# Kernel tuning notes

Hardware: AMD Instinct MI355X
Metric: run time of the kernel (lower is better)

Reference implementation:

```python
import jax, jax.numpy as jnp
import numpy as np

B, T, N, F = 4, 1, 12500, 64
C = 64        # spatial_hidden_dim (heads=1)
OUT = 64      # spatial_out_features
E = 1600000
NT = B * N    # total flattened nodes


def setup_inputs() -> dict:
    key = jax.random.key(0)
    ks = jax.random.split(key, 12)
    s = lambda d: 1.0 / np.sqrt(d)
    return {
        "x": jax.random.normal(ks[0], (B, T, N, F), jnp.float32),
        "edge_index": jax.random.randint(ks[1], (2, E), 0, NT, jnp.int64),
        "edge_attr": jax.random.uniform(ks[2], (E, 1), jnp.float32),
        "W_l": jax.random.normal(ks[3], (F, C), jnp.float32) * s(F),
        "b_l": jnp.zeros((C,), jnp.float32),
        "W_r": jax.random.normal(ks[4], (F, C), jnp.float32) * s(F),
        "b_r": jnp.zeros((C,), jnp.float32),
        "W_e": jax.random.normal(ks[5], (1, C), jnp.float32),
        "att": jax.random.normal(ks[6], (C,), jnp.float32) * s(C),
        "bias": jnp.zeros((C,), jnp.float32),
        "W_fc": jax.random.normal(ks[7], (C, OUT), jnp.float32) * s(C),
        "b_fc": jnp.zeros((OUT,), jnp.float32),
    }


def reference(x, edge_index, edge_attr, W_l, b_l, W_r, b_r, W_e, att, bias, W_fc, b_fc):
    Bx, Tx, Nx, Fx = x.shape
    x2 = x.reshape(Bx * Nx, Fx)                      # [NT, F] (requires T==1)
    xl = x2 @ W_l + b_l                              # [NT, C] source transform
    xr = x2 @ W_r + b_r                              # [NT, C] target transform
    src, dst = edge_index[0], edge_index[1]
    e = edge_attr @ W_e                              # [E, C] lin_edge (no bias)
    m = jax.nn.leaky_relu(xl[src] + xr[dst] + e, 0.2)  # [E, C]
    score = m @ att                                  # [E]
    # segment softmax over destination nodes
    smax = jax.lax.stop_gradient(jax.ops.segment_max(score, dst, num_segments=Bx * Nx))
    ex = jnp.exp(score - smax[dst])
    denom = jax.ops.segment_sum(ex, dst, num_segments=Bx * Nx)
    alpha = ex / denom[dst]                          # [E]
    agg = jax.ops.segment_sum(alpha[:, None] * xl[src], dst, num_segments=Bx * Nx)
    out = (agg + bias).reshape(Bx, Nx, -1)           # [B, N, C]
    return out @ W_fc + b_fc                         # [B, N, OUT]
```

## Files before the change

kernel.cpp:

```cpp
#include <hip/hip_runtime.h>
#include <math.h>

#define LRELU(v) ((v) >= 0.f ? (v) : 0.2f * (v))

#define NB_SHIFT 4
#define BKT_NODES 16
#define MAXB 768
#define MAX_NBKT 3200
#define BIN_CHUNK 16384
#define TR_BLOCKS 512

__device__ __forceinline__ unsigned short f32_to_bf16_rne(float f) {
    unsigned int b = __float_as_uint(f);
    b += 0x7FFFu + ((b >> 16) & 1u);
    return (unsigned short)(b >> 16);
}

__global__ void __launch_bounds__(256) k_prep(
    const float* __restrict__ x,
    const float* __restrict__ W_l, const float* __restrict__ b_l,
    const float* __restrict__ W_r, const float* __restrict__ b_r,
    unsigned short* __restrict__ xl16, float* __restrict__ xr,
    const int* __restrict__ ei, const float* __restrict__ ea,
    int* __restrict__ bcnt, int2* __restrict__ bucket,
    int NT, int E, int nbkt, int binBlocks)
{
    __shared__ __align__(16) char smem[33792];
    const int t = threadIdx.x;
    if ((int)blockIdx.x < binBlocks) {
        int* lh = (int*)smem;
        int* lb = lh + MAX_NBKT;
        const int e0 = (int)blockIdx.x * BIN_CHUNK;
        const int e1 = (e0 + BIN_CHUNK < E) ? e0 + BIN_CHUNK : E;
        const int n = e1 - e0;
        const int nv4 = n >> 2;
        const int4* d4 = (const int4*)(ei + E + e0);
        const int4* s4 = (const int4*)(ei + e0);
        const float4* a4 = (const float4*)(ea + e0);
        for (int i = t; i < nbkt; i += 256) lh[i] = 0;
        __syncthreads();
        for (int j = t; j < nv4; j += 256) {
            const int4 v = d4[j];
            atomicAdd(&lh[v.x >> NB_SHIFT], 1);
            atomicAdd(&lh[v.y >> NB_SHIFT], 1);
            atomicAdd(&lh[v.z >> NB_SHIFT], 1);
            atomicAdd(&lh[v.w >> NB_SHIFT], 1);
        }
        for (int j = e0 + (nv4 << 2) + t; j < e1; j += 256)
            atomicAdd(&lh[ei[E + j] >> NB_SHIFT], 1);
        __syncthreads();
        for (int i = t; i < nbkt; i += 256) {
            const int c = lh[i];
            lb[i] = c ? atomicAdd(&bcnt[i], c) : 0;
            lh[i] = 0;
        }
        __syncthreads();
        for (int j = t; j < nv4; j += 256) {
            const int4 dv = d4[j];
            const int4 sv = s4[j];
            const float4 av = a4[j];
            int bkt, pos;
            bkt = dv.x >> NB_SHIFT;
            pos = lb[bkt] + atomicAdd(&lh[bkt], 1);
            if (pos < MAXB) bucket[(size_t)bkt * MAXB + pos] =
                make_int2(__float_as_int(av.x), sv.x | ((dv.x & (BKT_NODES - 1)) << 16));
            bkt = dv.y >> NB_SHIFT;
            pos = lb[bkt] + atomicAdd(&lh[bkt], 1);
            if (pos < MAXB) bucket[(size_t)bkt * MAXB + pos] =
                make_int2(__float_as_int(av.y), sv.y | ((dv.y & (BKT_NODES - 1)) << 16));
            bkt = dv.z >> NB_SHIFT;
            pos = lb[bkt] + atomicAdd(&lh[bkt], 1);
            if (pos < MAXB) bucket[(size_t)bkt * MAXB + pos] =
                make_int2(__float_as_int(av.z), sv.z | ((dv.z & (BKT_NODES - 1)) << 16));
            bkt = dv.w >> NB_SHIFT;
            pos = lb[bkt] + atomicAdd(&lh[bkt], 1);
            if (pos < MAXB) bucket[(size_t)bkt * MAXB + pos] =
                make_int2(__float_as_int(av.w), sv.w | ((dv.w & (BKT_NODES - 1)) << 16));
        }
        for (int j = e0 + (nv4 << 2) + t; j < e1; j += 256) {
            const int dst = ei[E + j];
            const int bkt = dst >> NB_SHIFT;
            const int pos = lb[bkt] + atomicAdd(&lh[bkt], 1);
            if (pos < MAXB)
                bucket[(size_t)bkt * MAXB + pos] =
                    make_int2(__float_as_int(ea[j]), ei[j] | ((dst & (BKT_NODES - 1)) << 16));
        }
    } else {
        float* sWl = (float*)smem;
        float* sWr = sWl + 64 * 64;
        float* sx  = sWr + 64 * 64;
        for (int i = t; i < 64 * 64; i += 256) { sWl[i] = W_l[i]; sWr[i] = W_r[i]; }
        const float bl = b_l[t & 63];
        const float br = b_r[t & 63];
        const int nTiles = (NT + 3) / 4;
        const int ln = t & 63;
        const int nr = t >> 6;
        for (int tile = (int)blockIdx.x - binBlocks; tile < nTiles; tile += TR_BLOCKS) {
            __syncthreads();
            const int node0 = tile * 4;
            if (node0 * 64 + t < NT * 64) sx[t] = x[node0 * 64 + t];
            __syncthreads();
            const int node = node0 + nr;
            if (node < NT) {
                float sl = bl, sr = br;
                #pragma unroll
                for (int k = 0; k < 64; ++k) {
                    const float xv = sx[nr * 64 + k];
                    sl = fmaf(xv, sWl[k * 64 + ln], sl);
                    sr = fmaf(xv, sWr[k * 64 + ln], sr);
                }
                xl16[node * 64 + ln] = f32_to_bf16_rne(sl);
                xr[node * 64 + ln] = sr;
            }
        }
    }
}

__global__ void __launch_bounds__(256) k_fused(
    const int* __restrict__ bcnt, const int2* __restrict__ bucket,
    const unsigned short* __restrict__ xl16, const float* __restrict__ xr,
    const float* __restrict__ W_e, const float* __restrict__ att,
    const float* __restrict__ bias, float* __restrict__ agg, int NT)
{
    __shared__ unsigned short perm16[MAXB];
    __shared__ int hist[BKT_NODES], base[BKT_NODES], cur[BKT_NODES];
    const int t = threadIdx.x;
    const int lane = t & 63;
    const int w = t >> 6;
    const int hl = lane & 7;
    const int h = lane >> 3;
    const int b = blockIdx.x;
    const int2* gb = bucket + (size_t)b * MAXB;
    int cnt = bcnt[b];
    if (cnt > MAXB) cnt = MAXB;

    if (t < BKT_NODES) hist[t] = 0;
    __syncthreads();
    for (int i = t; i < cnt; i += 256)
        atomicAdd(&hist[(gb[i].y >> 16) & (BKT_NODES - 1)], 1);
    __syncthreads();
    if (t == 0) {
        int run = 0;
        #pragma unroll
        for (int l = 0; l < BKT_NODES; ++l) { base[l] = run; cur[l] = run; run += hist[l]; }
    }
    __syncthreads();
    for (int i = t; i < cnt; i += 256) {
        const int dl = (gb[i].y >> 16) & (BKT_NODES - 1);
        perm16[atomicAdd(&cur[dl], 1)] = (unsigned short)i;
    }
    __syncthreads();

    const float4 we0 = ((const float4*)W_e)[2 * hl];
    const float4 we1 = ((const float4*)W_e)[2 * hl + 1];
    const float4 at0 = ((const float4*)att)[2 * hl];
    const float4 at1 = ((const float4*)att)[2 * hl + 1];
    const float4 bv0 = ((const float4*)bias)[2 * hl];
    const float4 bv1 = ((const float4*)bias)[2 * hl + 1];

    #pragma unroll
    for (int k = 0; k < 4; ++k) {
        const int l = w * 4 + k;
        const int node = b * BKT_NODES + l;
        if (node >= NT) break;
        const int sbeg = base[l];
        const int scnt = hist[l];
        const float4 xr0 = ((const float4*)xr)[node * 16 + 2 * hl];
        const float4 xr1 = ((const float4*)xr)[node * 16 + 2 * hl + 1];
        float a0 = 0.f, a1 = 0.f, a2 = 0.f, a3 = 0.f;
        float a4 = 0.f, a5 = 0.f, a6 = 0.f, a7 = 0.f;
        float den = 0.f;
        for (int c0 = 0; c0 < scnt; c0 += 64) {
            const int i = c0 + lane;
            int2 my = make_int2(0, 0);
            if (i < scnt) my = gb[perm16[sbeg + i]];
            const int cc = (scnt - c0 < 64) ? scnt - c0 : 64;
            for (int tt = 0; tt < cc; tt += 8) {
                const int eidx = tt + h;
                const int srcl = __shfl(my.y, eidx) & 0xFFFF;
                const float eav = __int_as_float(__shfl(my.x, eidx));
                const bool act = eidx < cc;
                float x0 = 0.f, x1 = 0.f, x2 = 0.f, x3 = 0.f;
                float x4 = 0.f, x5 = 0.f, x6 = 0.f, x7 = 0.f;
                if (act) {
                    const uint4 xb = ((const uint4*)(xl16 + (size_t)srcl * 64))[hl];
                    x0 = __uint_as_float(xb.x << 16);
                    x1 = __uint_as_float(xb.x & 0xFFFF0000u);
                    x2 = __uint_as_float(xb.y << 16);
                    x3 = __uint_as_float(xb.y & 0xFFFF0000u);
                    x4 = __uint_as_float(xb.z << 16);
                    x5 = __uint_as_float(xb.z & 0xFFFF0000u);
                    x6 = __uint_as_float(xb.w << 16);
                    x7 = __uint_as_float(xb.w & 0xFFFF0000u);
                }
                float v0 = x0 + xr0.x + eav * we0.x;
                float v1 = x1 + xr0.y + eav * we0.y;
                float v2 = x2 + xr0.z + eav * we0.z;
                float v3 = x3 + xr0.w + eav * we0.w;
                float v4 = x4 + xr1.x + eav * we1.x;
                float v5 = x5 + xr1.y + eav * we1.y;
                float v6 = x6 + xr1.z + eav * we1.z;
                float v7 = x7 + xr1.w + eav * we1.w;
                v0 = LRELU(v0); v1 = LRELU(v1); v2 = LRELU(v2); v3 = LRELU(v3);
                v4 = LRELU(v4); v5 = LRELU(v5); v6 = LRELU(v6); v7 = LRELU(v7);
                float p = v0 * at0.x + v1 * at0.y + v2 * at0.z + v3 * at0.w
                        + v4 * at1.x + v5 * at1.y + v6 * at1.z + v7 * at1.w;
                p += __shfl_xor(p, 1);
                p += __shfl_xor(p, 2);
                p += __shfl_xor(p, 4);
                const float ex = act ? __expf(p) : 0.f;
                den += ex;
                a0 = fmaf(ex, x0, a0); a1 = fmaf(ex, x1, a1);
                a2 = fmaf(ex, x2, a2); a3 = fmaf(ex, x3, a3);
                a4 = fmaf(ex, x4, a4); a5 = fmaf(ex, x5, a5);
                a6 = fmaf(ex, x6, a6); a7 = fmaf(ex, x7, a7);
            }
        }
        #pragma unroll
        for (int o = 8; o < 64; o <<= 1) {
            a0 += __shfl_xor(a0, o); a1 += __shfl_xor(a1, o);
            a2 += __shfl_xor(a2, o); a3 += __shfl_xor(a3, o);
            a4 += __shfl_xor(a4, o); a5 += __shfl_xor(a5, o);
            a6 += __shfl_xor(a6, o); a7 += __shfl_xor(a7, o);
            den += __shfl_xor(den, o);
        }
        const float inv = (den > 0.f) ? 1.f / den : 0.f;
        if (h == 0) {
            float4 r0, r1;
            r0.x = fmaf(a0, inv, bv0.x); r0.y = fmaf(a1, inv, bv0.y);
            r0.z = fmaf(a2, inv, bv0.z); r0.w = fmaf(a3, inv, bv0.w);
            r1.x = fmaf(a4, inv, bv1.x); r1.y = fmaf(a5, inv, bv1.y);
            r1.z = fmaf(a6, inv, bv1.z); r1.w = fmaf(a7, inv, bv1.w);
            float4* arow = (float4*)(agg + (size_t)node * 64);
            arow[2 * hl] = r0;
            arow[2 * hl + 1] = r1;
        }
    }
}

__global__ void __launch_bounds__(256) k_out(
    const float* __restrict__ agg,
    const float* __restrict__ W_fc, const float* __restrict__ b_fc,
    float* __restrict__ out, int NT)
{
    __shared__ float sW[64 * 64];
    __shared__ float sa[4 * 64];
    const int t = threadIdx.x;
    for (int i = t; i < 64 * 64; i += 256) sW[i] = W_fc[i];
    const int node0 = blockIdx.x * 4;
    if (node0 * 64 + t < NT * 64) sa[t] = agg[node0 * 64 + t];
    __syncthreads();
    const int ln = t & 63;
    const int nr = t >> 6;
    const int node = node0 + nr;
    if (node < NT) {
        float s = b_fc[ln];
        #pragma unroll
        for (int k = 0; k < 64; ++k) s = fmaf(sa[nr * 64 + k], sW[k * 64 + ln], s);
        out[node * 64 + ln] = s;
    }
}

extern "C" void kernel_launch(void* const* d_in, const int* in_sizes, int n_in,
                              void* d_out, int out_size, void* d_ws, size_t ws_size,
                              hipStream_t stream) {
    const float* x    = (const float*)d_in[0];
    const int*   ei   = (const int*)d_in[1];
    const float* ea   = (const float*)d_in[2];
    const float* W_l  = (const float*)d_in[3];
    const float* b_l  = (const float*)d_in[4];
    const float* W_r  = (const float*)d_in[5];
    const float* b_r  = (const float*)d_in[6];
    const float* W_e  = (const float*)d_in[7];
    const float* att  = (const float*)d_in[8];
    const float* bias = (const float*)d_in[9];
    const float* W_fc = (const float*)d_in[10];
    const float* b_fc = (const float*)d_in[11];
    float* out = (float*)d_out;

    const int NT = in_sizes[0] / 64;
    const int E  = in_sizes[2];
    const int nbkt = (NT + BKT_NODES - 1) / BKT_NODES;

    unsigned short* xl16 = (unsigned short*)d_ws;
    float* xr    = (float*)(xl16 + (size_t)NT * 64);
    float* agg   = xr + (size_t)NT * 64;
    int2* bucket = (int2*)(agg + (size_t)NT * 64);
    int* bcnt    = (int*)(bucket + (size_t)nbkt * MAXB);

    const int binBlocks = (E + BIN_CHUNK - 1) / BIN_CHUNK;
    const int nodeBlocks = (NT + 3) / 4;

    hipMemsetAsync(bcnt, 0, (size_t)nbkt * sizeof(int), stream);
    k_prep<<<binBlocks + TR_BLOCKS, 256, 0, stream>>>(
        x, W_l, b_l, W_r, b_r, xl16, xr, ei, ea, bcnt, bucket,
        NT, E, nbkt, binBlocks);
    k_fused<<<nbkt, 256, 0, stream>>>(bcnt, bucket, xl16, xr, W_e, att,
                                      bias, agg, NT);
    k_out<<<nodeBlocks, 256, 0, stream>>>(agg, W_fc, b_fc, out, NT);
}
```

Before: 141.2 us.

## Pad bucket reservations to 8-entry granularity and store aggregates as bf16

Each binning block now reserves bucket slots rounded up to a multiple of 8 and fills the unused tail with sentinel entries (y=-1), which the fused kernel skips. This aligns each block's writes to 64-byte segments to cut partial-line write traffic, at the cost of larger reservations, so MAXB grows to 1024. The intermediate aggregate buffer is also stored as packed bf16 instead of fp32, halving its write and read traffic between the fused and output kernels at some precision loss.

```diff
diff --git a/kernel.cpp b/kernel.cpp
--- a/kernel.cpp
+++ b/kernel.cpp
@@ -5,7 +5,7 @@
 
 #define NB_SHIFT 4
 #define BKT_NODES 16
-#define MAXB 768
+#define MAXB 1024
 #define MAX_NBKT 3200
 #define BIN_CHUNK 16384
 #define TR_BLOCKS 512
@@ -14,6 +14,9 @@
     unsigned int b = __float_as_uint(f);
     b += 0x7FFFu + ((b >> 16) & 1u);
     return (unsigned short)(b >> 16);
+}
+__device__ __forceinline__ unsigned int pack_bf16x2(float lo, float hi) {
+    return (unsigned int)f32_to_bf16_rne(lo) | ((unsigned int)f32_to_bf16_rne(hi) << 16);
 }
 
 __global__ void __launch_bounds__(256) k_prep(
@@ -51,7 +54,7 @@
         __syncthreads();
         for (int i = t; i < nbkt; i += 256) {
             const int c = lh[i];
-            lb[i] = c ? atomicAdd(&bcnt[i], c) : 0;
+            lb[i] = c ? atomicAdd(&bcnt[i], (c + 7) & ~7) : 0;
             lh[i] = 0;
         }
         __syncthreads();
@@ -84,6 +87,16 @@
             if (pos < MAXB)
                 bucket[(size_t)bkt * MAXB + pos] =
                     make_int2(__float_as_int(ea[j]), ei[j] | ((dst & (BKT_NODES - 1)) << 16));
+        }
+        __syncthreads();
+        for (int i = t; i < nbkt; i += 256) {
+            const int c = lh[i];
+            if (c) {
+                const int res = (c + 7) & ~7;
+                int2* bb = bucket + (size_t)i * MAXB;
+                for (int p = lb[i] + c; p < lb[i] + res && p < MAXB; ++p)
+                    bb[p] = make_int2(0, -1);
+            }
         }
     } else {
         float* sWl = (float*)smem;
@@ -120,7 +133,7 @@
     const int* __restrict__ bcnt, const int2* __restrict__ bucket,
     const unsigned short* __restrict__ xl16, const float* __restrict__ xr,
     const float* __restrict__ W_e, const float* __restrict__ att,
-    const float* __restrict__ bias, float* __restrict__ agg, int NT)
+    const float* __restrict__ bias, unsigned short* __restrict__ agg16, int NT)
 {
     __shared__ unsigned short perm16[MAXB];
     __shared__ int hist[BKT_NODES], base[BKT_NODES], cur[BKT_NODES];
@@ -136,8 +149,10 @@
 
     if (t < BKT_NODES) hist[t] = 0;
     __syncthreads();
-    for (int i = t; i < cnt; i += 256)
-        atomicAdd(&hist[(gb[i].y >> 16) & (BKT_NODES - 1)], 1);
+    for (int i = t; i < cnt; i += 256) {
+        const int y = gb[i].y;
+        if (y >= 0) atomicAdd(&hist[(y >> 16) & (BKT_NODES - 1)], 1);
+    }
     __syncthreads();
     if (t == 0) {
         int run = 0;
@@ -146,8 +161,9 @@
     }
     __syncthreads();
     for (int i = t; i < cnt; i += 256) {
-        const int dl = (gb[i].y >> 16) & (BKT_NODES - 1);
-        perm16[atomicAdd(&cur[dl], 1)] = (unsigned short)i;
+        const int y = gb[i].y;
+        if (y >= 0)
+            perm16[atomicAdd(&cur[(y >> 16) & (BKT_NODES - 1)], 1)] = (unsigned short)i;
     }
     __syncthreads();
 
@@ -226,20 +242,18 @@
         }
         const float inv = (den > 0.f) ? 1.f / den : 0.f;
         if (h == 0) {
-            float4 r0, r1;
-            r0.x = fmaf(a0, inv, bv0.x); r0.y = fmaf(a1, inv, bv0.y);
-            r0.z = fmaf(a2, inv, bv0.z); r0.w = fmaf(a3, inv, bv0.w);
-            r1.x = fmaf(a4, inv, bv1.x); r1.y = fmaf(a5, inv, bv1.y);
-            r1.z = fmaf(a6, inv, bv1.z); r1.w = fmaf(a7, inv, bv1.w);
-            float4* arow = (float4*)(agg + (size_t)node * 64);
-            arow[2 * hl] = r0;
-            arow[2 * hl + 1] = r1;
+            uint4 r;
+            r.x = pack_bf16x2(fmaf(a0, inv, bv0.x), fmaf(a1, inv, bv0.y));
+            r.y = pack_bf16x2(fmaf(a2, inv, bv0.z), fmaf(a3, inv, bv0.w));
+            r.z = pack_bf16x2(fmaf(a4, inv, bv1.x), fmaf(a5, inv, bv1.y));
+            r.w = pack_bf16x2(fmaf(a6, inv, bv1.z), fmaf(a7, inv, bv1.w));
+            ((uint4*)(agg16 + (size_t)node * 64))[hl] = r;
         }
     }
 }
 
 __global__ void __launch_bounds__(256) k_out(
-    const float* __restrict__ agg,
+    const unsigned short* __restrict__ agg16,
     const float* __restrict__ W_fc, const float* __restrict__ b_fc,
     float* __restrict__ out, int NT)
 {
@@ -248,7 +262,11 @@
     const int t = threadIdx.x;
     for (int i = t; i < 64 * 64; i += 256) sW[i] = W_fc[i];
     const int node0 = blockIdx.x * 4;
-    if (node0 * 64 + t < NT * 64) sa[t] = agg[node0 * 64 + t];
+    if (t < 128 && node0 * 64 + 2 * t < NT * 64) {
+        const unsigned int v = ((const unsigned int*)agg16)[node0 * 32 + t];
+        sa[2 * t]     = __uint_as_float(v << 16);
+        sa[2 * t + 1] = __uint_as_float(v & 0xFFFF0000u);
+    }
     __syncthreads();
     const int ln = t & 63;
     const int nr = t >> 6;
@@ -284,8 +302,8 @@
 
     unsigned short* xl16 = (unsigned short*)d_ws;
     float* xr    = (float*)(xl16 + (size_t)NT * 64);
-    float* agg   = xr + (size_t)NT * 64;
-    int2* bucket = (int2*)(agg + (size_t)NT * 64);
+    unsigned short* agg16 = (unsigned short*)(xr + (size_t)NT * 64);
+    int2* bucket = (int2*)(agg16 + (size_t)NT * 64);
     int* bcnt    = (int*)(bucket + (size_t)nbkt * MAXB);
 
     const int binBlocks = (E + BIN_CHUNK - 1) / BIN_CHUNK;
@@ -296,6 +314,6 @@
         x, W_l, b_l, W_r, b_r, xl16, xr, ei, ea, bcnt, bucket,
         NT, E, nbkt, binBlocks);
     k_fused<<<nbkt, 256, 0, stream>>>(bcnt, bucket, xl16, xr, W_e, att,
-                                      bias, agg, NT);
-    k_out<<<nodeBlocks, 256, 0, stream>>>(agg, W_fc, b_fc, out, NT);
-}
+                                      bias, agg16, NT);
+    k_out<<<nodeBlocks, 256, 0, stream>>>(agg16, W_fc, b_fc, out, NT);
+}
```

Measured after the change: 150.2 us. 1.06x slower.
